# Performance work log

Hardware: AMD Instinct MI355X
Metric: run time of the kernel (lower is better)

Reference implementation:

```python
import jax, jax.numpy as jnp
import numpy as np

N_HEADS = 12
HEAD_DIM = 64
EMB = 768


def setup_inputs() -> dict:
    key = jax.random.key(0)
    k1, k2, k3 = jax.random.split(key, 3)
    B, S = 4, 2048
    x = jax.random.normal(k1, (B, S, EMB), dtype=jnp.float32)
    # nn.Linear-style init scale ~ 1/sqrt(fan_in)
    w_qkv = jax.random.normal(k2, (EMB, 3 * N_HEADS * HEAD_DIM), dtype=jnp.float32) * (EMB ** -0.5)
    w_out = jax.random.normal(k3, (N_HEADS * HEAD_DIM, EMB), dtype=jnp.float32) * ((N_HEADS * HEAD_DIM) ** -0.5)
    b_out = jnp.zeros((EMB,), dtype=jnp.float32)
    return {"x": x, "w_qkv": w_qkv, "w_out": w_out, "b_out": b_out}


def reference(x, w_qkv, w_out, b_out):
    B, S, E = x.shape
    qkv = x @ w_qkv                                   # [B,S,3*H*D]
    q, k, v = jnp.split(qkv, 3, axis=-1)
    def to_heads(t):
        return t.reshape(B, S, N_HEADS, HEAD_DIM).transpose(0, 2, 1, 3)  # [B,H,S,D]
    q, k, v = to_heads(q), to_heads(k), to_heads(v)
    scores = jnp.einsum('bhqd,bhkd->bhqk', q, k) / (HEAD_DIM ** 0.5)     # [B,H,S,S]
    probs = jax.nn.softmax(scores, axis=-1)
    attn = jnp.einsum('bhqk,bhkd->bhqd', probs, v)                       # [B,H,S,D]
    attn = attn.transpose(0, 2, 1, 3).reshape(B, S, N_HEADS * HEAD_DIM)
    return attn @ w_out + b_out
```

## Files before the change

kernel.cpp:

```cpp
#include <hip/hip_runtime.h>
#include <stdint.h>

typedef unsigned short u16;
typedef __attribute__((ext_vector_type(8))) __bf16 bf16x8;
typedef __attribute__((ext_vector_type(4))) __bf16 bf16x4;
typedef __attribute__((ext_vector_type(8))) unsigned short u16x8;
typedef __attribute__((ext_vector_type(4))) float f32x4;

__device__ __forceinline__ void glds16(const u16* g, u16* l) {
  auto* gp = reinterpret_cast<const __attribute__((address_space(1))) unsigned*>(
      reinterpret_cast<uintptr_t>(g));
  auto* lp = reinterpret_cast<__attribute__((address_space(3))) unsigned*>(
      reinterpret_cast<uintptr_t>(l));
  __builtin_amdgcn_global_load_lds(gp, lp, 16, 0, 0);
}

__device__ __forceinline__ void tp_tile(const float* __restrict__ src,
                                        u16* __restrict__ dst, int C, int Rd,
                                        int r0, int c0, u16* lds) {
  const int tid = threadIdx.x;
  {
    int r = tid >> 2, cb = (tid & 3) * 16;
#pragma unroll
    for (int k = 0; k < 4; ++k) {
      f32x4 v = *(const f32x4*)&src[(long)(r0 + r) * C + c0 + cb + k * 4];
      *(bf16x4*)&lds[r * 72 + cb + k * 4] = __builtin_convertvector(v, bf16x4);
    }
  }
  __syncthreads();
  {
    int c = tid >> 2, rb = (tid & 3) * 16;
    u16x8 o0, o1;
#pragma unroll
    for (int q = 0; q < 8; ++q) {
      o0[q] = lds[(rb + q) * 72 + c];
      o1[q] = lds[(rb + 8 + q) * 72 + c];
    }
    *(u16x8*)&dst[(long)(c0 + c) * Rd + r0 + rb] = o0;
    *(u16x8*)&dst[(long)(c0 + c) * Rd + r0 + rb + 8] = o1;
  }
}

__global__ __launch_bounds__(256) void prep_k(const float* __restrict__ w_qkv,
                                              const float* __restrict__ w_out,
                                              const float* __restrict__ x,
                                              u16* __restrict__ wqkvT,
                                              u16* __restrict__ woutT,
                                              u16* __restrict__ xb) {
  __shared__ u16 lds[64 * 72];
  int bx = blockIdx.x;
  if (bx < 432) {
    int tr = bx / 36, tc = bx % 36;
    tp_tile(w_qkv, wqkvT, 2304, 768, tr * 64, tc * 64, lds);
  } else if (bx < 576) {
    int t = bx - 432;
    tp_tile(w_out, woutT, 768, 768, (t / 12) * 64, (t % 12) * 64, lds);
  } else {
    int base = ((bx - 576) * 256 + (int)threadIdx.x) * 8;
#pragma unroll
    for (int it = 0; it < 16; ++it, base += 393216) {
      f32x4 a = *(const f32x4*)&x[base];
      f32x4 b = *(const f32x4*)&x[base + 4];
      *(bf16x4*)&xb[base] = __builtin_convertvector(a, bf16x4);
      *(bf16x4*)&xb[base + 4] = __builtin_convertvector(b, bf16x4);
    }
  }
}

template <bool OF32>
__device__ __forceinline__ void gemm_core(const u16* __restrict__ A,
                                          const u16* __restrict__ BT,
                                          void* __restrict__ Cv,
                                          const float* __restrict__ bias,
                                          int N, int K, int br, int bc,
                                          u16* As, u16* Bs) {
  const int tid = threadIdx.x;
  const int lane = tid & 63, wave = tid >> 6;
  const int quad = lane >> 4, l16 = lane & 15;
  const int wm = (wave >> 1) * 64, wn = (wave & 1) * 64;

  f32x4 acc[4][4] = {};

  const int srow = wave * 32 + (lane >> 2);
  const int scol = ((lane & 3) ^ ((lane >> 3) & 3)) * 8;
  const u16* ag = A + (long)(br + srow) * K + scol;
  const u16* bg = BT + (long)(bc + srow) * K + scol;
  const int rd = (quad ^ ((l16 >> 1) & 3)) * 8;

  for (int k0 = 0; k0 < K; k0 += 32) {
    glds16(ag + k0, As + wave * 1024);
    glds16(ag + k0 + 16 * K, As + wave * 1024 + 512);
    glds16(bg + k0, Bs + wave * 1024);
    glds16(bg + k0 + 16 * K, Bs + wave * 1024 + 512);
    __syncthreads();
    bf16x8 af[4], bf[4];
#pragma unroll
    for (int i = 0; i < 4; ++i)
      af[i] = *(const bf16x8*)&As[(wm + i * 16 + l16) * 32 + rd];
#pragma unroll
    for (int j = 0; j < 4; ++j)
      bf[j] = *(const bf16x8*)&Bs[(wn + j * 16 + l16) * 32 + rd];
#pragma unroll
    for (int i = 0; i < 4; ++i)
#pragma unroll
      for (int j = 0; j < 4; ++j)
        acc[i][j] = __builtin_amdgcn_mfma_f32_16x16x32_bf16(af[i], bf[j],
                                                            acc[i][j], 0, 0, 0);
    __syncthreads();
  }

#pragma unroll
  for (int i = 0; i < 4; ++i)
#pragma unroll
    for (int j = 0; j < 4; ++j)
#pragma unroll
      for (int r = 0; r < 4; ++r) {
        int row = br + wm + i * 16 + quad * 4 + r;
        int col = bc + wn + j * 16 + l16;
        float v = acc[i][j][r];
        if (OF32) {
          ((float*)Cv)[(long)row * N + col] = v + bias[col];
        } else {
          ((__bf16*)Cv)[(long)row * N + col] = (__bf16)v;
        }
      }
}

__global__ __launch_bounds__(256) void qkvt_k(const u16* __restrict__ xb,
                                              const u16* __restrict__ wqkvT,
                                              u16* __restrict__ qk,
                                              u16* __restrict__ vt) {
  __shared__ __align__(16) u16 As[128 * 32];
  __shared__ __align__(16) u16 Bs[128 * 32];
  int bx = blockIdx.x;
  if (bx < 768) {
    gemm_core<false>(xb, wqkvT, qk, nullptr, 1536, 768, (bx / 12) * 128,
                     (bx % 12) * 128, As, Bs);
  } else {
    int i = bx - 768;
    gemm_core<false>(wqkvT + 1536 * 768, xb, vt, nullptr, 8192, 768,
                     (i >> 6) * 128, (i & 63) * 128, As, Bs);
  }
}

__global__ __launch_bounds__(256) void gemm2_k(const u16* __restrict__ attnb,
                                               const u16* __restrict__ woutT,
                                               float* __restrict__ out,
                                               const float* __restrict__ bias) {
  __shared__ __align__(16) u16 As[128 * 32];
  __shared__ __align__(16) u16 Bs[128 * 32];
  gemm_core<true>(attnb, woutT, out, bias, 768, 768, blockIdx.y * 128,
                  blockIdx.x * 128, As, Bs);
}

__global__ __launch_bounds__(256, 4) void attn_k(const u16* __restrict__ qk,
                                                 const u16* __restrict__ vt,
                                                 u16* __restrict__ attnb) {
  const int LQ = 72;
  __shared__ __align__(16) u16 Ks[64 * 64];
  __shared__ __align__(16) u16 Vs[64 * 64];
  __shared__ __align__(16) u16 Ps[128 * LQ];

  const int tid = threadIdx.x;
  const int lane = tid & 63, wave = tid >> 6;
  const int quad = lane >> 4, l16 = lane & 15;
  const int bid = blockIdx.x;
  const int xcd = bid & 7, slot = bid >> 3;
  const int bh = xcd * 6 + (slot >> 4);
  const int qt = slot & 15;
  const int bloc = bh / 12, h = bh % 12;
  const long rowbase = (long)bloc * 2048;

#pragma unroll
  for (int it = 0; it < 4; ++it) {
    int c = tid + it * 256;
    int m = c >> 3, off = (c & 7) * 8;
    *(u16x8*)&Ps[m * LQ + off] =
        *(const u16x8*)&qk[(rowbase + qt * 128 + m) * 1536 + h * 64 + off];
  }
  __syncthreads();

  bf16x8 aq[2][2];
#pragma unroll
  for (int kk = 0; kk < 2; ++kk)
#pragma unroll
    for (int i = 0; i < 2; ++i)
      aq[kk][i] = *(const bf16x8*)&Ps[(wave * 32 + i * 16 + l16) * LQ +
                                      kk * 32 + quad * 8];

  bf16x8 ones;
#pragma unroll
  for (int q = 0; q < 8; ++q) ones[q] = (__bf16)1.0f;

  const int trow = lane >> 3;
  const int tcol = ((lane & 7) ^ trow) * 8;
  const u16* kg = qk + (rowbase + wave * 16 + trow) * 1536 + 768 + h * 64 + tcol;
  const u16* vg = vt + (long)(h * 64 + wave * 16 + trow) * 8192 + rowbase + tcol;
  u16* kl = Ks + wave * 1024;
  u16* vl = Vs + wave * 1024;
  const int sw = l16 & 7;

  f32x4 o[2][4] = {};
  f32x4 l_acc[2] = {};

  for (int t = 0; t < 32; ++t) {
    const long kvK = (long)t * 64 * 1536;
    const long kvV = (long)t * 64;
    glds16(kg + kvK, kl);
    glds16(kg + kvK + 8 * 1536, kl + 512);
    glds16(vg + kvV, vl);
    glds16(vg + kvV + 8 * 8192, vl + 512);
    __syncthreads();

    f32x4 sc[4][2] = {};
#pragma unroll
    for (int kk = 0; kk < 2; ++kk) {
      bf16x8 bk[4];
#pragma unroll
      for (int j = 0; j < 4; ++j)
        bk[j] = *(const bf16x8*)&Ks[(j * 16 + l16) * 64 +
                                    ((kk * 4 + quad) ^ sw) * 8];
#pragma unroll
      for (int j = 0; j < 4; ++j)
#pragma unroll
        for (int i = 0; i < 2; ++i)
          sc[j][i] = __builtin_amdgcn_mfma_f32_16x16x32_bf16(bk[j], aq[kk][i],
                                                             sc[j][i], 0, 0, 0);
    }

#pragma unroll
    for (int i = 0; i < 2; ++i)
#pragma unroll
      for (int j = 0; j < 4; ++j) {
        f32x4 p;
#pragma unroll
        for (int r = 0; r < 4; ++r)
          p[r] = exp2f(sc[j][i][r] * 0.18033688011112042f);
        *(bf16x4*)&Ps[(wave * 32 + i * 16 + l16) * LQ + j * 16 + quad * 4] =
            __builtin_convertvector(p, bf16x4);
      }

#pragma unroll
    for (int kk = 0; kk < 2; ++kk) {
      bf16x8 ap[2], bv[4];
#pragma unroll
      for (int i = 0; i < 2; ++i)
        ap[i] = *(const bf16x8*)&Ps[(wave * 32 + i * 16 + l16) * LQ + kk * 32 +
                                    quad * 8];
#pragma unroll
      for (int n = 0; n < 4; ++n)
        bv[n] = *(const bf16x8*)&Vs[(n * 16 + l16) * 64 +
                                    ((kk * 4 + quad) ^ sw) * 8];
#pragma unroll
      for (int i = 0; i < 2; ++i) {
        l_acc[i] = __builtin_amdgcn_mfma_f32_16x16x32_bf16(ones, ap[i],
                                                           l_acc[i], 0, 0, 0);
#pragma unroll
        for (int n = 0; n < 4; ++n)
          o[i][n] = __builtin_amdgcn_mfma_f32_16x16x32_bf16(ap[i], bv[n],
                                                            o[i][n], 0, 0, 0);
      }
    }
    __syncthreads();
  }

#pragma unroll
  for (int i = 0; i < 2; ++i) {
    f32x4 inv;
#pragma unroll
    for (int r = 0; r < 4; ++r)
      inv[r] = 1.0f / __shfl(l_acc[i][0], quad * 4 + r, 64);
#pragma unroll
    for (int n = 0; n < 4; ++n)
#pragma unroll
      for (int r = 0; r < 4; ++r) {
        int srow = qt * 128 + wave * 32 + i * 16 + quad * 4 + r;
        ((__bf16*)attnb)[(rowbase + srow) * 768 + h * 64 + n * 16 + l16] =
            (__bf16)(o[i][n][r] * inv[r]);
      }
  }
}

extern "C" void kernel_launch(void* const* d_in, const int* in_sizes, int n_in,
                              void* d_out, int out_size, void* d_ws,
                              size_t ws_size, hipStream_t stream) {
  const float* x = (const float*)d_in[0];
  const float* w_qkv = (const float*)d_in[1];
  const float* w_out = (const float*)d_in[2];
  const float* b_out = (const float*)d_in[3];
  float* out = (float*)d_out;

  char* ws = (char*)d_ws;
  u16* wqkvT = (u16*)(ws);
  u16* woutT = (u16*)(ws + 3538944);
  u16* vt = (u16*)(ws + 4718592);
  u16* xb = (u16*)(ws + 17301504);
  u16* attnb = xb;
  u16* qkb = (u16*)d_out;

  prep_k<<<768, 256, 0, stream>>>(w_qkv, w_out, x, wqkvT, woutT, xb);
  qkvt_k<<<1152, 256, 0, stream>>>(xb, wqkvT, qkb, vt);
  attn_k<<<768, 256, 0, stream>>>(qkb, vt, attnb);
  gemm2_k<<<dim3(6, 64), 256, 0, stream>>>(attnb, woutT, out, b_out);
}
```

Before: 242.2 us.

## Split attention KV tile across wave pairs and fold softmax scale into Q weights

Reorganizes attention waves so each pair of waves covers 64 query rows and splits the 64-key tile in halves, so K/V fragments are reused across four query sub-tiles per wave. Partial O and row sums from the two key halves are combined through shared memory at the end. The softmax scale is folded into the Q columns of the QKV weight during the prep transpose, which removes a multiply per score. The cost is more accumulator registers, which lowers the occupancy hint from 4 to 3, plus an extra reduction pass through LDS.

```diff
diff --git a/kernel.cpp b/kernel.cpp
--- a/kernel.cpp
+++ b/kernel.cpp
@@ -17,13 +17,14 @@
 
 __device__ __forceinline__ void tp_tile(const float* __restrict__ src,
                                         u16* __restrict__ dst, int C, int Rd,
-                                        int r0, int c0, u16* lds) {
+                                        int r0, int c0, float scale, u16* lds) {
   const int tid = threadIdx.x;
   {
     int r = tid >> 2, cb = (tid & 3) * 16;
 #pragma unroll
     for (int k = 0; k < 4; ++k) {
       f32x4 v = *(const f32x4*)&src[(long)(r0 + r) * C + c0 + cb + k * 4];
+      v = v * scale;
       *(bf16x4*)&lds[r * 72 + cb + k * 4] = __builtin_convertvector(v, bf16x4);
     }
   }
@@ -51,10 +52,11 @@
   int bx = blockIdx.x;
   if (bx < 432) {
     int tr = bx / 36, tc = bx % 36;
-    tp_tile(w_qkv, wqkvT, 2304, 768, tr * 64, tc * 64, lds);
+    float sc = (tc < 12) ? 0.18033688011112042f : 1.0f;
+    tp_tile(w_qkv, wqkvT, 2304, 768, tr * 64, tc * 64, sc, lds);
   } else if (bx < 576) {
     int t = bx - 432;
-    tp_tile(w_out, woutT, 768, 768, (t / 12) * 64, (t % 12) * 64, lds);
+    tp_tile(w_out, woutT, 768, 768, (t / 12) * 64, (t % 12) * 64, 1.0f, lds);
   } else {
     int base = ((bx - 576) * 256 + (int)threadIdx.x) * 8;
 #pragma unroll
@@ -153,17 +155,19 @@
                   blockIdx.x * 128, As, Bs);
 }
 
-__global__ __launch_bounds__(256, 4) void attn_k(const u16* __restrict__ qk,
+__global__ __launch_bounds__(256, 3) void attn_k(const u16* __restrict__ qk,
                                                  const u16* __restrict__ vt,
                                                  u16* __restrict__ attnb) {
   const int LQ = 72;
-  __shared__ __align__(16) u16 Ks[64 * 64];
-  __shared__ __align__(16) u16 Vs[64 * 64];
-  __shared__ __align__(16) u16 Ps[128 * LQ];
+  __shared__ __align__(16) u16 smem[17408];
+  u16* Ks = smem;
+  u16* Vs = smem + 4096;
+  u16* Ps = smem + 8192;
 
   const int tid = threadIdx.x;
   const int lane = tid & 63, wave = tid >> 6;
   const int quad = lane >> 4, l16 = lane & 15;
+  const int qh = wave >> 1, sh = wave & 1;
   const int bid = blockIdx.x;
   const int xcd = bid & 7, slot = bid >> 3;
   const int bh = xcd * 6 + (slot >> 4);
@@ -180,13 +184,13 @@
   }
   __syncthreads();
 
-  bf16x8 aq[2][2];
+  bf16x8 aq[2][4];
 #pragma unroll
   for (int kk = 0; kk < 2; ++kk)
 #pragma unroll
-    for (int i = 0; i < 2; ++i)
-      aq[kk][i] = *(const bf16x8*)&Ps[(wave * 32 + i * 16 + l16) * LQ +
-                                      kk * 32 + quad * 8];
+    for (int i = 0; i < 4; ++i)
+      aq[kk][i] = *(const bf16x8*)&Ps[(qh * 64 + i * 16 + l16) * LQ + kk * 32 +
+                                      quad * 8];
 
   bf16x8 ones;
 #pragma unroll
@@ -200,8 +204,8 @@
   u16* vl = Vs + wave * 1024;
   const int sw = l16 & 7;
 
-  f32x4 o[2][4] = {};
-  f32x4 l_acc[2] = {};
+  f32x4 o[4][4] = {};
+  f32x4 l_acc[4] = {};
 
   for (int t = 0; t < 32; ++t) {
     const long kvK = (long)t * 64 * 1536;
@@ -212,72 +216,85 @@
     glds16(vg + kvV + 8 * 8192, vl + 512);
     __syncthreads();
 
-    f32x4 sc[4][2] = {};
-#pragma unroll
-    for (int kk = 0; kk < 2; ++kk) {
-      bf16x8 bk[4];
-#pragma unroll
-      for (int j = 0; j < 4; ++j)
-        bk[j] = *(const bf16x8*)&Ks[(j * 16 + l16) * 64 +
-                                    ((kk * 4 + quad) ^ sw) * 8];
-#pragma unroll
-      for (int j = 0; j < 4; ++j)
-#pragma unroll
-        for (int i = 0; i < 2; ++i)
-          sc[j][i] = __builtin_amdgcn_mfma_f32_16x16x32_bf16(bk[j], aq[kk][i],
-                                                             sc[j][i], 0, 0, 0);
-    }
-
-#pragma unroll
-    for (int i = 0; i < 2; ++i)
-#pragma unroll
-      for (int j = 0; j < 4; ++j) {
+#pragma unroll
+    for (int j = 0; j < 2; ++j) {
+      bf16x8 bk0 = *(const bf16x8*)&Ks[(sh * 32 + j * 16 + l16) * 64 +
+                                       ((0 * 4 + quad) ^ sw) * 8];
+      bf16x8 bk1 = *(const bf16x8*)&Ks[(sh * 32 + j * 16 + l16) * 64 +
+                                       ((1 * 4 + quad) ^ sw) * 8];
+      f32x4 sc[4] = {};
+#pragma unroll
+      for (int i = 0; i < 4; ++i) {
+        sc[i] = __builtin_amdgcn_mfma_f32_16x16x32_bf16(bk0, aq[0][i], sc[i],
+                                                        0, 0, 0);
+        sc[i] = __builtin_amdgcn_mfma_f32_16x16x32_bf16(bk1, aq[1][i], sc[i],
+                                                        0, 0, 0);
+      }
+#pragma unroll
+      for (int i = 0; i < 4; ++i) {
         f32x4 p;
 #pragma unroll
-        for (int r = 0; r < 4; ++r)
-          p[r] = exp2f(sc[j][i][r] * 0.18033688011112042f);
-        *(bf16x4*)&Ps[(wave * 32 + i * 16 + l16) * LQ + j * 16 + quad * 4] =
-            __builtin_convertvector(p, bf16x4);
+        for (int r = 0; r < 4; ++r) p[r] = exp2f(sc[i][r]);
+        *(bf16x4*)&Ps[(qh * 64 + i * 16 + l16) * LQ + sh * 32 + j * 16 +
+                      quad * 4] = __builtin_convertvector(p, bf16x4);
       }
-
-#pragma unroll
-    for (int kk = 0; kk < 2; ++kk) {
-      bf16x8 ap[2], bv[4];
-#pragma unroll
-      for (int i = 0; i < 2; ++i)
-        ap[i] = *(const bf16x8*)&Ps[(wave * 32 + i * 16 + l16) * LQ + kk * 32 +
-                                    quad * 8];
+    }
+
+    {
+      bf16x8 bv[4];
 #pragma unroll
       for (int n = 0; n < 4; ++n)
         bv[n] = *(const bf16x8*)&Vs[(n * 16 + l16) * 64 +
-                                    ((kk * 4 + quad) ^ sw) * 8];
-#pragma unroll
-      for (int i = 0; i < 2; ++i) {
-        l_acc[i] = __builtin_amdgcn_mfma_f32_16x16x32_bf16(ones, ap[i],
-                                                           l_acc[i], 0, 0, 0);
+                                    ((sh * 4 + quad) ^ sw) * 8];
+#pragma unroll
+      for (int i = 0; i < 4; ++i) {
+        bf16x8 ap = *(const bf16x8*)&Ps[(qh * 64 + i * 16 + l16) * LQ +
+                                        sh * 32 + quad * 8];
+        l_acc[i] = __builtin_amdgcn_mfma_f32_16x16x32_bf16(ones, ap, l_acc[i],
+                                                           0, 0, 0);
 #pragma unroll
         for (int n = 0; n < 4; ++n)
-          o[i][n] = __builtin_amdgcn_mfma_f32_16x16x32_bf16(ap[i], bv[n],
-                                                            o[i][n], 0, 0, 0);
+          o[i][n] = __builtin_amdgcn_mfma_f32_16x16x32_bf16(ap, bv[n], o[i][n],
+                                                            0, 0, 0);
       }
     }
     __syncthreads();
   }
 
-#pragma unroll
-  for (int i = 0; i < 2; ++i) {
-    f32x4 inv;
-#pragma unroll
-    for (int r = 0; r < 4; ++r)
-      inv[r] = 1.0f / __shfl(l_acc[i][0], quad * 4 + r, 64);
-#pragma unroll
-    for (int n = 0; n < 4; ++n)
-#pragma unroll
-      for (int r = 0; r < 4; ++r) {
-        int srow = qt * 128 + wave * 32 + i * 16 + quad * 4 + r;
-        ((__bf16*)attnb)[(rowbase + srow) * 768 + h * 64 + n * 16 + l16] =
-            (__bf16)(o[i][n][r] * inv[r]);
-      }
+  float* Of = (float*)smem;
+  float* Lp = (float*)&smem[16384];
+  if (sh == 1) {
+#pragma unroll
+    for (int i = 0; i < 4; ++i) {
+#pragma unroll
+      for (int n = 0; n < 4; ++n)
+#pragma unroll
+        for (int r = 0; r < 4; ++r)
+          Of[(qh * 64 + i * 16 + quad * 4 + r) * 64 + n * 16 + l16] =
+              o[i][n][r];
+      if (quad == 0) Lp[qh * 64 + i * 16 + l16] = l_acc[i][0];
+    }
+  }
+  __syncthreads();
+  if (sh == 0) {
+#pragma unroll
+    for (int i = 0; i < 4; ++i) {
+      float lsum = l_acc[i][0] + Lp[qh * 64 + i * 16 + l16];
+      f32x4 inv;
+#pragma unroll
+      for (int r = 0; r < 4; ++r)
+        inv[r] = 1.0f / __shfl(lsum, quad * 4 + r, 64);
+#pragma unroll
+      for (int n = 0; n < 4; ++n)
+#pragma unroll
+        for (int r = 0; r < 4; ++r) {
+          int srow = qt * 128 + qh * 64 + i * 16 + quad * 4 + r;
+          float v = o[i][n][r] +
+                    Of[(qh * 64 + i * 16 + quad * 4 + r) * 64 + n * 16 + l16];
+          ((__bf16*)attnb)[(rowbase + srow) * 768 + h * 64 + n * 16 + l16] =
+              (__bf16)(v * inv[r]);
+        }
+    }
   }
 }
 
```

Result: faster. 229.2 us (-5.4%).
